# Kernel tuning notes

Hardware: AMD Instinct MI355X
Metric: run time of the kernel (lower is better)

## Reference

```python
import jax, jax.numpy as jnp
import numpy as np

EMBED_DIM = 1024
N_HEADS = 16
HEAD_DIM = EMBED_DIM // N_HEADS


def setup_inputs() -> dict:
    key = jax.random.key(0)
    k_x, k_wqkv, k_bqkv, k_wo, k_bo = jax.random.split(key, 5)
    s = 1.0 / np.sqrt(EMBED_DIM)
    return {
        "x": jax.random.normal(k_x, (2, 2048, EMBED_DIM), dtype=jnp.float32),
        "w_qkv": jax.random.uniform(k_wqkv, (EMBED_DIM, 3 * EMBED_DIM), jnp.float32, -s, s),
        "b_qkv": jax.random.uniform(k_bqkv, (3 * EMBED_DIM,), jnp.float32, -s, s),
        "w_out": jax.random.uniform(k_wo, (EMBED_DIM, EMBED_DIM), jnp.float32, -s, s),
        "b_out": jax.random.uniform(k_bo, (EMBED_DIM,), jnp.float32, -s, s),
    }


def reference(x, w_qkv, b_qkv, w_out, b_out):
    B, T, C = x.shape
    qkv = x @ w_qkv + b_qkv                      # [B,T,3C]
    q, k, v = jnp.split(qkv, 3, axis=-1)
    # [B,T,C] -> [B,H,T,D]
    def heads(t):
        return t.reshape(B, T, N_HEADS, HEAD_DIM).transpose(0, 2, 1, 3)
    q, k, v = heads(q), heads(k), heads(v)
    scale = 1.0 / np.sqrt(HEAD_DIM).astype(np.float32)
    scores = jnp.einsum("bhqd,bhkd->bhqk", q, k) * scale
    causal = jnp.tril(jnp.ones((T, T), dtype=bool))  # True where allowed
    scores = jnp.where(causal, scores, jnp.finfo(scores.dtype).min)
    attn = jax.nn.softmax(scores, axis=-1)
    out = jnp.einsum("bhqk,bhkd->bhqd", attn, v)
    out = out.transpose(0, 2, 1, 3).reshape(B, T, C)
    return out @ w_out + b_out
```

## Files before the change

### kernel.cpp

```cpp
#include <hip/hip_runtime.h>
#include <hip/hip_bf16.h>

typedef __attribute__((ext_vector_type(4))) float f32x4;
typedef __attribute__((ext_vector_type(8))) short bf16x8;

static __device__ __forceinline__ unsigned short f2bf(float f) {
  union { float f; unsigned u; } v;
  v.f = f;
  unsigned r = v.u + 0x7FFFu + ((v.u >> 16) & 1u);
  return (unsigned short)(r >> 16);
}

static __device__ __forceinline__ void gload16(const void* g, void* lds) {
  __builtin_amdgcn_global_load_lds(
      (const __attribute__((address_space(1))) unsigned int*)g,
      (__attribute__((address_space(3))) unsigned int*)lds, 16, 0, 0);
}

__global__ __launch_bounds__(256) void prep_kernel(
    const float* __restrict__ x, const float* __restrict__ w_qkv,
    const float* __restrict__ w_out, unsigned short* __restrict__ xb,
    unsigned short* __restrict__ wqkvT, unsigned short* __restrict__ woT) {
  __shared__ float tile[32][33];
  const int bid = blockIdx.x, tid = threadIdx.x;
  if (bid < 4096) {
    int i = bid * 256 + tid;
    float4 v = reinterpret_cast<const float4*>(x)[i];
    ushort4 o;
    o.x = f2bf(v.x); o.y = f2bf(v.y); o.z = f2bf(v.z); o.w = f2bf(v.w);
    reinterpret_cast<ushort4*>(xb)[i] = o;
    return;
  }
  const float* src; unsigned short* dst; int c0, r0, C;
  if (bid < 7168) {
    int t = bid - 4096;
    src = w_qkv; dst = wqkvT; C = 3072;
    c0 = (t % 96) * 32; r0 = (t / 96) * 32;
  } else {
    int t = bid - 7168;
    src = w_out; dst = woT; C = 1024;
    c0 = (t & 31) * 32; r0 = (t >> 5) * 32;
  }
  int tx = tid & 31, ty = tid >> 5;
#pragma unroll
  for (int i = 0; i < 32; i += 8)
    tile[ty + i][tx] = src[(size_t)(r0 + ty + i) * C + c0 + tx];
  __syncthreads();
#pragma unroll
  for (int i = 0; i < 32; i += 8)
    dst[(size_t)(c0 + ty + i) * 1024 + r0 + tx] = f2bf(tile[tx][ty + i]);
}

template <int MODE, int BN>
__global__ __launch_bounds__(256) void gemm_bf16(
    const unsigned short* __restrict__ A,
    const unsigned short* __restrict__ Bt,
    const float* __restrict__ bias,
    unsigned short* __restrict__ q_out,
    unsigned short* __restrict__ k_out,
    unsigned short* __restrict__ v_out,
    float* __restrict__ f_out) {
  constexpr int NB2 = BN / 32;
  constexpr int NBL = BN / 64;
  __shared__ __align__(16) unsigned short As[2][128 * 32];
  __shared__ __align__(16) unsigned short Bs[2][BN * 32];

  const int tid = threadIdx.x;
  const int wid = tid >> 6, lane = tid & 63;
  const int l15 = lane & 15, g = lane >> 4;
  const int wm = wid >> 1, wn = wid & 1;
  const int n0 = blockIdx.x * BN, m0 = blockIdx.y * 128;

  f32x4 acc[4][NB2] = {};

  auto stage = [&](int k0, int bsel) {
#pragma unroll
    for (int i = 0; i < 2; ++i) {
      int t = tid + i * 256;
      int row = t >> 2, c8 = (t & 3) << 3;
      gload16(A + (size_t)(m0 + row) * 1024 + k0 + c8, &As[bsel][(i * 256 + wid * 64) * 8]);
    }
#pragma unroll
    for (int i = 0; i < NBL; ++i) {
      int t = tid + i * 256;
      int row = t >> 2, c8 = (t & 3) << 3;
      gload16(Bt + (size_t)(n0 + row) * 1024 + k0 + c8, &Bs[bsel][(i * 256 + wid * 64) * 8]);
    }
  };

  stage(0, 0);
  __syncthreads();
  for (int ks = 0; ks < 32; ++ks) {
    const int cur = ks & 1;
    if (ks + 1 < 32) stage((ks + 1) * 32, cur ^ 1);
    bf16x8 a[4], b[NB2];
#pragma unroll
    for (int mi = 0; mi < 4; ++mi)
      a[mi] = *reinterpret_cast<const bf16x8*>(&As[cur][(wm * 64 + mi * 16 + l15) * 32 + g * 8]);
#pragma unroll
    for (int ni = 0; ni < NB2; ++ni)
      b[ni] = *reinterpret_cast<const bf16x8*>(&Bs[cur][(wn * (BN / 2) + ni * 16 + l15) * 32 + g * 8]);
    __builtin_amdgcn_s_setprio(1);
#pragma unroll
    for (int mi = 0; mi < 4; ++mi)
#pragma unroll
      for (int ni = 0; ni < NB2; ++ni)
        acc[mi][ni] = __builtin_amdgcn_mfma_f32_16x16x32_bf16(a[mi], b[ni], acc[mi][ni], 0, 0, 0);
    __builtin_amdgcn_s_setprio(0);
    __syncthreads();
  }

  if (MODE == 0) {
    const int which = n0 >> 10;
    unsigned short* dst = (which == 0) ? q_out : (which == 1) ? k_out : v_out;
#pragma unroll
    for (int ni = 0; ni < NB2; ++ni) {
      int col = n0 + wn * (BN / 2) + ni * 16 + l15;
      int c = col & 1023;
      int h = c >> 6, d = c & 63;
      float bv = bias[col];
#pragma unroll
      for (int mi = 0; mi < 4; ++mi) {
#pragma unroll
        for (int r = 0; r < 4; ++r) {
          int rowg = m0 + wm * 64 + mi * 16 + g * 4 + r;
          int bb = rowg >> 11, tt = rowg & 2047;
          dst[((bb * 16 + h) * 2048 + tt) * 64 + d] = f2bf(acc[mi][ni][r] + bv);
        }
      }
    }
  } else {
#pragma unroll
    for (int ni = 0; ni < NB2; ++ni) {
      int col = n0 + wn * (BN / 2) + ni * 16 + l15;
      float bv = bias[col];
#pragma unroll
      for (int mi = 0; mi < 4; ++mi)
#pragma unroll
        for (int r = 0; r < 4; ++r) {
          int rowg = m0 + wm * 64 + mi * 16 + g * 4 + r;
          f_out[(size_t)rowg * 1024 + col] = acc[mi][ni][r] + bv;
        }
    }
  }
}

#define KS_SZ (64 * 64)
#define VT_SZ (64 * 72)

__device__ __forceinline__ void attn_stage_K(const unsigned short* __restrict__ Kb,
                                             int k0, unsigned short* KsBuf,
                                             int tid, int wid) {
#pragma unroll
  for (int i = 0; i < 2; ++i) {
    int t = tid + i * 256;
    int row = t >> 3;
    int cb = (t & 7) << 4;
    int src = cb ^ ((row & 7) << 4);
    gload16((const char*)Kb + (size_t)(k0 + row) * 128 + src,
            (char*)KsBuf + (i * 256 + wid * 64) * 16);
  }
}

__device__ __forceinline__ void write_vt(unsigned short* VtBuf, int kvL, int d8,
                                         bf16x8 va, bf16x8 vb) {
#pragma unroll
  for (int j = 0; j < 8; ++j) {
    unsigned pk = (unsigned)(unsigned short)va[j] |
                  ((unsigned)(unsigned short)vb[j] << 16);
    *reinterpret_cast<unsigned*>(&VtBuf[(d8 + j) * 72 + kvL]) = pk;
  }
}

__device__ __forceinline__ void attn_run_qtile(
    const unsigned short* __restrict__ Qb,
    const unsigned short* __restrict__ Kb,
    const unsigned short* __restrict__ Vb,
    unsigned short* __restrict__ O,
    int b, int h, int q0, int nt,
    unsigned short* Ks, unsigned short* Vt, unsigned short* Ps,
    int tid, int wid, int l15, int g) {
  const float SC = 0.125f * 1.44269504f;

  bf16x8 qf[2];
  {
    const unsigned short* qrow = Qb + (size_t)(q0 + wid * 16 + l15) * 64;
    qf[0] = *reinterpret_cast<const bf16x8*>(qrow + g * 8);
    qf[1] = *reinterpret_cast<const bf16x8*>(qrow + 32 + g * 8);
  }

  float m_run = -1e30f, l_run = 0.0f;
  f32x4 ot[4] = {};
  const int qg = q0 + wid * 16 + l15;
  const int kvL = (tid & 31) * 2, d8 = (tid >> 5) * 8;
  const int qrow = wid * 16 + l15;

  attn_stage_K(Kb, 0, Ks, tid, wid);
  {
    const unsigned short* vp = Vb + (size_t)kvL * 64 + d8;
    bf16x8 va = *reinterpret_cast<const bf16x8*>(vp);
    bf16x8 vb = *reinterpret_cast<const bf16x8*>(vp + 64);
    write_vt(Vt, kvL, d8, va, vb);
  }
  __syncthreads();

  for (int t = 0; t < nt; ++t) {
    const unsigned short* KsC = Ks + (t & 1) * KS_SZ;
    const unsigned short* VtC = Vt + (t & 1) * VT_SZ;
    bf16x8 va, vb;
    const bool pf = (t + 1 < nt);
    if (pf) {
      attn_stage_K(Kb, (t + 1) << 6, Ks + ((t + 1) & 1) * KS_SZ, tid, wid);
      const unsigned short* vp = Vb + (size_t)(((t + 1) << 6) + kvL) * 64 + d8;
      va = *reinterpret_cast<const bf16x8*>(vp);
      vb = *reinterpret_cast<const bf16x8*>(vp + 64);
    }

    f32x4 s[4] = {};
    __builtin_amdgcn_s_setprio(1);
#pragma unroll
    for (int kk = 0; kk < 2; ++kk)
#pragma unroll
      for (int mi = 0; mi < 4; ++mi) {
        int row = mi * 16 + l15;
        int cb = (kk * 64 + g * 16) ^ ((row & 7) << 4);
        bf16x8 kf = *reinterpret_cast<const bf16x8*>((const char*)KsC + row * 128 + cb);
        s[mi] = __builtin_amdgcn_mfma_f32_16x16x32_bf16(kf, qf[kk], s[mi], 0, 0, 0);
      }
    __builtin_amdgcn_s_setprio(0);

    float tmax = -1e30f;
    if (t == nt - 1) {
      const int k0 = t << 6;
#pragma unroll
      for (int mi = 0; mi < 4; ++mi)
#pragma unroll
        for (int r = 0; r < 4; ++r) {
          int kvg = k0 + mi * 16 + g * 4 + r;
          float sv = s[mi][r] * SC;
          sv = (kvg <= qg) ? sv : -1e30f;
          s[mi][r] = sv;
          tmax = fmaxf(tmax, sv);
        }
    } else {
#pragma unroll
      for (int mi = 0; mi < 4; ++mi)
#pragma unroll
        for (int r = 0; r < 4; ++r) {
          float sv = s[mi][r] * SC;
          s[mi][r] = sv;
          tmax = fmaxf(tmax, sv);
        }
    }
    tmax = fmaxf(tmax, __shfl_xor(tmax, 16));
    tmax = fmaxf(tmax, __shfl_xor(tmax, 32));

    if (!__all(tmax <= m_run + 8.0f)) {
      float m_new = fmaxf(m_run, tmax);
      float corr = __builtin_amdgcn_exp2f(m_run - m_new);
      l_run *= corr;
#pragma unroll
      for (int mi = 0; mi < 4; ++mi)
#pragma unroll
        for (int r = 0; r < 4; ++r) ot[mi][r] *= corr;
      m_run = m_new;
    }

    float tsum = 0.f;
#pragma unroll
    for (int mi = 0; mi < 4; ++mi) {
#pragma unroll
      for (int r2 = 0; r2 < 2; ++r2) {
        float p0 = __builtin_amdgcn_exp2f(s[mi][2 * r2] - m_run);
        float p1 = __builtin_amdgcn_exp2f(s[mi][2 * r2 + 1] - m_run);
        tsum += p0 + p1;
        unsigned pk = (unsigned)f2bf(p0) | ((unsigned)f2bf(p1) << 16);
        *reinterpret_cast<unsigned*>(&Ps[qrow * 72 + mi * 16 + g * 4 + 2 * r2]) = pk;
      }
    }
    tsum += __shfl_xor(tsum, 16);
    tsum += __shfl_xor(tsum, 32);
    l_run += tsum;

    __builtin_amdgcn_s_setprio(1);
#pragma unroll
    for (int kk = 0; kk < 2; ++kk) {
      bf16x8 pfr = *reinterpret_cast<const bf16x8*>(Ps + qrow * 72 + kk * 32 + g * 8);
#pragma unroll
      for (int mi = 0; mi < 4; ++mi) {
        bf16x8 vf = *reinterpret_cast<const bf16x8*>(VtC + (mi * 16 + l15) * 72 + kk * 32 + g * 8);
        ot[mi] = __builtin_amdgcn_mfma_f32_16x16x32_bf16(vf, pfr, ot[mi], 0, 0, 0);
      }
    }
    __builtin_amdgcn_s_setprio(0);

    if (pf) write_vt(Vt + ((t + 1) & 1) * VT_SZ, kvL, d8, va, vb);
    __syncthreads();
  }

  float inv_l = 1.0f / l_run;
#pragma unroll
  for (int mi = 0; mi < 4; ++mi)
#pragma unroll
    for (int r = 0; r < 4; ++r) {
      int d = mi * 16 + g * 4 + r;
      int cb = (d * 2) ^ ((qrow & 7) << 4);
      *reinterpret_cast<unsigned short*>((char*)Ks + qrow * 128 + cb) = f2bf(ot[mi][r] * inv_l);
    }
  __syncthreads();
#pragma unroll
  for (int i = 0; i < 2; ++i) {
    int t = tid + i * 256;
    int row = t >> 3;
    int cb = (t & 7) << 4;
    int sw = cb ^ ((row & 7) << 4);
    bf16x8 vv = *reinterpret_cast<const bf16x8*>((const char*)Ks + row * 128 + sw);
    *reinterpret_cast<bf16x8*>(O + ((size_t)(b * 2048 + q0 + row)) * 1024 + h * 64 + (cb >> 1)) = vv;
  }
  __syncthreads();
}

__global__ __launch_bounds__(256) void attn_fwd(
    const unsigned short* __restrict__ Q,
    const unsigned short* __restrict__ K,
    const unsigned short* __restrict__ V,
    unsigned short* __restrict__ O) {
  __shared__ __align__(16) unsigned short Ks[2 * KS_SZ];
  __shared__ __align__(16) unsigned short Vt[2 * VT_SZ];
  __shared__ __align__(16) unsigned short Ps[64 * 72];

  const int tid = threadIdx.x;
  const int wid = tid >> 6;
  const int l15 = tid & 15;
  const int g = (tid & 63) >> 4;

  int lin = blockIdx.x + (blockIdx.y << 4);
  int w = ((lin & 7) << 6) + (lin >> 3);
  const int pi = w & 15, bh = w >> 4;
  const int b = bh >> 4, h = bh & 15;

  const unsigned short* Qb = Q + (size_t)bh * 2048 * 64;
  const unsigned short* Kb = K + (size_t)bh * 2048 * 64;
  const unsigned short* Vb = V + (size_t)bh * 2048 * 64;

  attn_run_qtile(Qb, Kb, Vb, O, b, h, pi << 6, pi + 1, Ks, Vt, Ps, tid, wid, l15, g);
  attn_run_qtile(Qb, Kb, Vb, O, b, h, (31 - pi) << 6, 32 - pi, Ks, Vt, Ps, tid, wid, l15, g);
}

extern "C" void kernel_launch(void* const* d_in, const int* in_sizes, int n_in,
                              void* d_out, int out_size, void* d_ws, size_t ws_size,
                              hipStream_t stream) {
  const float* x = (const float*)d_in[0];
  const float* w_qkv = (const float*)d_in[1];
  const float* b_qkv = (const float*)d_in[2];
  const float* w_out = (const float*)d_in[3];
  const float* b_out = (const float*)d_in[4];
  float* out = (float*)d_out;
  char* ws = (char*)d_ws;

  unsigned short* xb    = (unsigned short*)d_out;
  unsigned short* wqkvT = (unsigned short*)(ws);
  unsigned short* woT   = (unsigned short*)(ws + 6291456);
  unsigned short* q_buf = (unsigned short*)(ws + 8388608);
  unsigned short* k_buf = (unsigned short*)(ws + 16777216);
  unsigned short* v_buf = (unsigned short*)(ws + 25165824);
  unsigned short* aout  = (unsigned short*)(ws + 33554432);

  prep_kernel<<<dim3(8192), dim3(256), 0, stream>>>(x, w_qkv, w_out, xb, wqkvT, woT);

  gemm_bf16<0, 128><<<dim3(24, 32), dim3(256), 0, stream>>>(
      xb, wqkvT, b_qkv, q_buf, k_buf, v_buf, nullptr);

  attn_fwd<<<dim3(16, 32), dim3(256), 0, stream>>>(q_buf, k_buf, v_buf, aout);

  gemm_bf16<1, 64><<<dim3(16, 32), dim3(256), 0, stream>>>(
      aout, woT, b_out, nullptr, nullptr, nullptr, out);
}
```

Before: 121.1 us.

## Fold softmax scale into Q projection and streamline attention inner loop

Moves the softmax scale and log2e factor into the Q projection epilogue, which removes the per-score multiply in attention. The row-max shuffle now runs only when a rescale is needed, and the row-sum shuffle is deferred to the end. V transpose packing uses byte-permute instructions, and bf16 packing uses the hardware v_cvt_pk_bf16_f32 with wider LDS stores. Launch-bound occupancy hints are also added to the GEMM and attention kernels. Bf16 rounding of Q now happens after scaling, which changes numerics slightly, and the occupancy hints may force register spills.

Measured after the change: 107.0 us. 11.6% less time.

```diff
diff --git a/kernel.cpp b/kernel.cpp
--- a/kernel.cpp
+++ b/kernel.cpp
@@ -9,6 +9,12 @@
   v.f = f;
   unsigned r = v.u + 0x7FFFu + ((v.u >> 16) & 1u);
   return (unsigned short)(r >> 16);
+}
+
+static __device__ __forceinline__ unsigned cvt_pk_bf16(float lo, float hi) {
+  unsigned r;
+  asm("v_cvt_pk_bf16_f32 %0, %1, %2" : "=v"(r) : "v"(lo), "v"(hi));
+  return r;
 }
 
 static __device__ __forceinline__ void gload16(const void* g, void* lds) {
@@ -52,7 +58,7 @@
 }
 
 template <int MODE, int BN>
-__global__ __launch_bounds__(256) void gemm_bf16(
+__global__ __launch_bounds__(256, MODE == 0 ? 3 : 2) void gemm_bf16(
     const unsigned short* __restrict__ A,
     const unsigned short* __restrict__ Bt,
     const float* __restrict__ bias,
@@ -113,6 +119,7 @@
   if (MODE == 0) {
     const int which = n0 >> 10;
     unsigned short* dst = (which == 0) ? q_out : (which == 1) ? k_out : v_out;
+    const float oscale = (which == 0) ? 0.125f * 1.44269504f : 1.0f;
 #pragma unroll
     for (int ni = 0; ni < NB2; ++ni) {
       int col = n0 + wn * (BN / 2) + ni * 16 + l15;
@@ -125,7 +132,7 @@
         for (int r = 0; r < 4; ++r) {
           int rowg = m0 + wm * 64 + mi * 16 + g * 4 + r;
           int bb = rowg >> 11, tt = rowg & 2047;
-          dst[((bb * 16 + h) * 2048 + tt) * 64 + d] = f2bf(acc[mi][ni][r] + bv);
+          dst[((bb * 16 + h) * 2048 + tt) * 64 + d] = f2bf((acc[mi][ni][r] + bv) * oscale);
         }
       }
     }
@@ -163,13 +170,21 @@
 }
 
 __device__ __forceinline__ void write_vt(unsigned short* VtBuf, int kvL, int d8,
-                                         bf16x8 va, bf16x8 vb) {
-#pragma unroll
-  for (int j = 0; j < 8; ++j) {
-    unsigned pk = (unsigned)(unsigned short)va[j] |
-                  ((unsigned)(unsigned short)vb[j] << 16);
-    *reinterpret_cast<unsigned*>(&VtBuf[(d8 + j) * 72 + kvL]) = pk;
-  }
+                                         uint4 v0, uint4 v1) {
+  unsigned* base = reinterpret_cast<unsigned*>(&VtBuf[(size_t)d8 * 72 + kvL]);
+  unsigned lo, hi;
+  lo = __builtin_amdgcn_perm(v1.x, v0.x, 0x05040100u);
+  hi = __builtin_amdgcn_perm(v1.x, v0.x, 0x07060302u);
+  base[0] = lo;   base[36] = hi;
+  lo = __builtin_amdgcn_perm(v1.y, v0.y, 0x05040100u);
+  hi = __builtin_amdgcn_perm(v1.y, v0.y, 0x07060302u);
+  base[72] = lo;  base[108] = hi;
+  lo = __builtin_amdgcn_perm(v1.z, v0.z, 0x05040100u);
+  hi = __builtin_amdgcn_perm(v1.z, v0.z, 0x07060302u);
+  base[144] = lo; base[180] = hi;
+  lo = __builtin_amdgcn_perm(v1.w, v0.w, 0x05040100u);
+  hi = __builtin_amdgcn_perm(v1.w, v0.w, 0x07060302u);
+  base[216] = lo; base[252] = hi;
 }
 
 __device__ __forceinline__ void attn_run_qtile(
@@ -180,16 +195,15 @@
     int b, int h, int q0, int nt,
     unsigned short* Ks, unsigned short* Vt, unsigned short* Ps,
     int tid, int wid, int l15, int g) {
-  const float SC = 0.125f * 1.44269504f;
-
   bf16x8 qf[2];
   {
-    const unsigned short* qrow = Qb + (size_t)(q0 + wid * 16 + l15) * 64;
-    qf[0] = *reinterpret_cast<const bf16x8*>(qrow + g * 8);
-    qf[1] = *reinterpret_cast<const bf16x8*>(qrow + 32 + g * 8);
-  }
-
-  float m_run = -1e30f, l_run = 0.0f;
+    const unsigned short* qrow_p = Qb + (size_t)(q0 + wid * 16 + l15) * 64;
+    qf[0] = *reinterpret_cast<const bf16x8*>(qrow_p + g * 8);
+    qf[1] = *reinterpret_cast<const bf16x8*>(qrow_p + 32 + g * 8);
+  }
+
+  float m_run = -1e30f;
+  float l_run = 0.0f;
   f32x4 ot[4] = {};
   const int qg = q0 + wid * 16 + l15;
   const int kvL = (tid & 31) * 2, d8 = (tid >> 5) * 8;
@@ -197,23 +211,22 @@
 
   attn_stage_K(Kb, 0, Ks, tid, wid);
   {
-    const unsigned short* vp = Vb + (size_t)kvL * 64 + d8;
-    bf16x8 va = *reinterpret_cast<const bf16x8*>(vp);
-    bf16x8 vb = *reinterpret_cast<const bf16x8*>(vp + 64);
-    write_vt(Vt, kvL, d8, va, vb);
+    const uint4* vp = reinterpret_cast<const uint4*>(Vb + (size_t)kvL * 64 + d8);
+    write_vt(Vt, kvL, d8, vp[0], vp[8]);
   }
   __syncthreads();
 
   for (int t = 0; t < nt; ++t) {
     const unsigned short* KsC = Ks + (t & 1) * KS_SZ;
     const unsigned short* VtC = Vt + (t & 1) * VT_SZ;
-    bf16x8 va, vb;
+    uint4 va, vb;
     const bool pf = (t + 1 < nt);
     if (pf) {
       attn_stage_K(Kb, (t + 1) << 6, Ks + ((t + 1) & 1) * KS_SZ, tid, wid);
-      const unsigned short* vp = Vb + (size_t)(((t + 1) << 6) + kvL) * 64 + d8;
-      va = *reinterpret_cast<const bf16x8*>(vp);
-      vb = *reinterpret_cast<const bf16x8*>(vp + 64);
+      const uint4* vp = reinterpret_cast<const uint4*>(
+          Vb + (size_t)(((t + 1) << 6) + kvL) * 64 + d8);
+      va = vp[0];
+      vb = vp[8];
     }
 
     f32x4 s[4] = {};
@@ -229,7 +242,6 @@
       }
     __builtin_amdgcn_s_setprio(0);
 
-    float tmax = -1e30f;
     if (t == nt - 1) {
       const int k0 = t << 6;
 #pragma unroll
@@ -237,25 +249,19 @@
 #pragma unroll
         for (int r = 0; r < 4; ++r) {
           int kvg = k0 + mi * 16 + g * 4 + r;
-          float sv = s[mi][r] * SC;
-          sv = (kvg <= qg) ? sv : -1e30f;
-          s[mi][r] = sv;
-          tmax = fmaxf(tmax, sv);
+          s[mi][r] = (kvg <= qg) ? s[mi][r] : -1e30f;
         }
-    } else {
-#pragma unroll
-      for (int mi = 0; mi < 4; ++mi)
-#pragma unroll
-        for (int r = 0; r < 4; ++r) {
-          float sv = s[mi][r] * SC;
-          s[mi][r] = sv;
-          tmax = fmaxf(tmax, sv);
-        }
-    }
-    tmax = fmaxf(tmax, __shfl_xor(tmax, 16));
-    tmax = fmaxf(tmax, __shfl_xor(tmax, 32));
-
-    if (!__all(tmax <= m_run + 8.0f)) {
+    }
+
+    float pmax = -1e30f;
+#pragma unroll
+    for (int mi = 0; mi < 4; ++mi)
+#pragma unroll
+      for (int r = 0; r < 4; ++r) pmax = fmaxf(pmax, s[mi][r]);
+
+    if (!__all(pmax <= m_run + 8.0f)) {
+      float tmax = fmaxf(pmax, __shfl_xor(pmax, 16));
+      tmax = fmaxf(tmax, __shfl_xor(tmax, 32));
       float m_new = fmaxf(m_run, tmax);
       float corr = __builtin_amdgcn_exp2f(m_run - m_new);
       l_run *= corr;
@@ -269,17 +275,16 @@
     float tsum = 0.f;
 #pragma unroll
     for (int mi = 0; mi < 4; ++mi) {
-#pragma unroll
-      for (int r2 = 0; r2 < 2; ++r2) {
-        float p0 = __builtin_amdgcn_exp2f(s[mi][2 * r2] - m_run);
-        float p1 = __builtin_amdgcn_exp2f(s[mi][2 * r2 + 1] - m_run);
-        tsum += p0 + p1;
-        unsigned pk = (unsigned)f2bf(p0) | ((unsigned)f2bf(p1) << 16);
-        *reinterpret_cast<unsigned*>(&Ps[qrow * 72 + mi * 16 + g * 4 + 2 * r2]) = pk;
-      }
-    }
-    tsum += __shfl_xor(tsum, 16);
-    tsum += __shfl_xor(tsum, 32);
+      float p0 = __builtin_amdgcn_exp2f(s[mi][0] - m_run);
+      float p1 = __builtin_amdgcn_exp2f(s[mi][1] - m_run);
+      float p2 = __builtin_amdgcn_exp2f(s[mi][2] - m_run);
+      float p3 = __builtin_amdgcn_exp2f(s[mi][3] - m_run);
+      tsum += (p0 + p1) + (p2 + p3);
+      uint2 pk;
+      pk.x = cvt_pk_bf16(p0, p1);
+      pk.y = cvt_pk_bf16(p2, p3);
+      *reinterpret_cast<uint2*>((char*)Ps + qrow * 144 + mi * 32 + g * 8) = pk;
+    }
     l_run += tsum;
 
     __builtin_amdgcn_s_setprio(1);
@@ -298,15 +303,18 @@
     __syncthreads();
   }
 
-  float inv_l = 1.0f / l_run;
-#pragma unroll
-  for (int mi = 0; mi < 4; ++mi)
-#pragma unroll
-    for (int r = 0; r < 4; ++r) {
-      int d = mi * 16 + g * 4 + r;
-      int cb = (d * 2) ^ ((qrow & 7) << 4);
-      *reinterpret_cast<unsigned short*>((char*)Ks + qrow * 128 + cb) = f2bf(ot[mi][r] * inv_l);
-    }
+  float l_tot = l_run + __shfl_xor(l_run, 16);
+  l_tot += __shfl_xor(l_tot, 32);
+  float inv_l = 1.0f / l_tot;
+
+#pragma unroll
+  for (int mi = 0; mi < 4; ++mi) {
+    uint2 pk;
+    pk.x = cvt_pk_bf16(ot[mi][0] * inv_l, ot[mi][1] * inv_l);
+    pk.y = cvt_pk_bf16(ot[mi][2] * inv_l, ot[mi][3] * inv_l);
+    int b0 = (mi * 32 + g * 8) ^ ((qrow & 7) << 4);
+    *reinterpret_cast<uint2*>((char*)Ks + qrow * 128 + b0) = pk;
+  }
   __syncthreads();
 #pragma unroll
   for (int i = 0; i < 2; ++i) {
@@ -320,7 +328,7 @@
   __syncthreads();
 }
 
-__global__ __launch_bounds__(256) void attn_fwd(
+__global__ __launch_bounds__(256, 2) void attn_fwd(
     const unsigned short* __restrict__ Q,
     const unsigned short* __restrict__ K,
     const unsigned short* __restrict__ V,
```
